# Optimization experiments

Hardware: AMD Instinct MI355X
Metric: run time of the kernel (lower is better)

Reference implementation:

```python
import jax, jax.numpy as jnp
import numpy as np

VOCAB = 50257
EMB = 512


def setup_inputs() -> dict:
    key = jax.random.key(0)
    k1, k2, k3 = jax.random.split(key, 3)
    input_token_ids = jax.random.randint(k1, (8, 4096), 0, VOCAB, dtype=jnp.int64 if jax.config.jax_enable_x64 else jnp.int32)
    W = jax.random.normal(k2, (EMB, VOCAB), dtype=jnp.float32)  # nn.Linear(vocab, emb).weight
    b = jax.random.normal(k3, (EMB,), dtype=jnp.float32)        # nn.Linear bias
    return {"input_token_ids": input_token_ids, "W": W, "b": b}


def reference(input_token_ids, W, b):
    # one_hot(ids, V) @ W.T + b  ==  W.T[ids] + b   (exact same math, gather form)
    scale = jnp.asarray(EMB, W.dtype) ** 0.5
    emb = jnp.take(W.T, input_token_ids, axis=0)  # [B, S, EMB]
    return (emb + b) * scale
```

## Files before the change

kernel.cpp:

```cpp
#include <hip/hip_runtime.h>


constexpr int VOCAB = 50257;
constexpr int EMB   = 512;
constexpr int NTOK  = 8 * 4096;
constexpr float SCALE = 22.62741699796952f;

constexpr int VB   = 256;
constexpr int NB   = (VOCAB + VB - 1) / VB;
constexpr int CAP  = 256;
constexpr int ECH  = 64;
constexpr int RSD  = VB + 1;
constexpr int SMEM_BYTES = (ECH * RSD + CAP) * 4;


__global__ __launch_bounds__(256) void build_buckets(
    const int* __restrict__ ids,
    int* __restrict__ counts,
    int* __restrict__ olist,
    int* __restrict__ buckets)
{
    int t = blockIdx.x * 256 + threadIdx.x;
    int id = ids[t];
    int bkt = id >> 8;
    int slot = atomicAdd(&counts[bkt], 1);
    if (slot < CAP) {
        buckets[bkt * CAP + slot] = (t << 8) | (id & 255);
    } else {
        int o = atomicAdd(&counts[NB], 1);
        olist[o] = t;
    }
}

__global__ __launch_bounds__(512) void scatter_main(
    const float* __restrict__ W,
    const float* __restrict__ bias,
    const int*   __restrict__ counts,
    const int*   __restrict__ buckets,
    const int*   __restrict__ olist,
    const int*   __restrict__ ids,
    float*       __restrict__ out)
{
    extern __shared__ float smem[];
    float* tile = smem;
    int*   toks = (int*)(smem + ECH * RSD);

    const int bid  = blockIdx.x;
    const int b    = bid >> 3;
    const int ec   = bid & 7;
    const int e0   = ec * ECH;
    const int tid  = threadIdx.x;
    const int lane = tid & 63;
    const int w    = tid >> 6;

    const int vstart = min(b * VB, VOCAB - VB);
    const int vadj   = b * VB - vstart;

    const int cnt = min(counts[b], CAP);
    if (tid < CAP) toks[tid] = buckets[b * CAP + tid];
    const float be = bias[e0 + lane];

    #pragma unroll
    for (int p = 0; p < 8; ++p) {
        const int r = w * 8 + p;
        const size_t rowbase = (size_t)(e0 + r) * VOCAB + vstart;
        #pragma unroll
        for (int q = 0; q < 4; ++q) {
            const float* gp = W + rowbase + q * 64 + lane;
            float* lp = &tile[r * RSD + q * 64];
            __builtin_amdgcn_global_load_lds(
                (const __attribute__((address_space(1))) void*)gp,
                (__attribute__((address_space(3))) void*)lp, 4, 0, 0);
        }
    }
    __syncthreads();

    const float* tl   = &tile[lane * RSD];
    float*       outp = out + e0 + lane;
    for (int i = w; i < cnt; i += 8) {
        const int pk = toks[i];
        const int t  = pk >> 8;
        const int vl = (pk & 255) + vadj;
        outp[(size_t)t * EMB] = (tl[vl] + be) * SCALE;
    }

    if (b == 0) {
        int n = counts[NB];
        for (int ww = w; ww < n; ww += 8) {
            int t  = olist[ww];
            int id = ids[t];
            int e  = e0 + lane;
            out[(size_t)t * EMB + e] = (W[(size_t)e * VOCAB + id] + bias[e]) * SCALE;
        }
    }
}

__global__ __launch_bounds__(256) void embed_gather(
    const int*   __restrict__ ids,
    const float* __restrict__ W,
    const float* __restrict__ b,
    float*       __restrict__ out)
{
    int idx4 = blockIdx.x * blockDim.x + threadIdx.x;
    int t    = idx4 >> 7;
    int e    = (idx4 & 127) << 2;
    int id = ids[t];
    float4 bb = *reinterpret_cast<const float4*>(b + e);
    const float* wcol = W + (size_t)id;
    float4 o;
    o.x = (wcol[(size_t)(e + 0) * VOCAB] + bb.x) * SCALE;
    o.y = (wcol[(size_t)(e + 1) * VOCAB] + bb.y) * SCALE;
    o.z = (wcol[(size_t)(e + 2) * VOCAB] + bb.z) * SCALE;
    o.w = (wcol[(size_t)(e + 3) * VOCAB] + bb.w) * SCALE;
    *reinterpret_cast<float4*>(out + (size_t)idx4 * 4) = o;
}

extern "C" void kernel_launch(void* const* d_in, const int* in_sizes, int n_in,
                              void* d_out, int out_size, void* d_ws, size_t ws_size,
                              hipStream_t stream)
{
    const int*   ids  = (const int*)  d_in[0];
    const float* W    = (const float*)d_in[1];
    const float* bias = (const float*)d_in[2];
    float*       out  = (float*)d_out;

    const size_t ws_ints_needed = (size_t)NB + 1 + NTOK + (size_t)NB * CAP;

    if (ws_size >= ws_ints_needed * sizeof(int)) {
        int* counts  = (int*)d_ws;
        int* olist   = counts + NB + 1;
        int* buckets = olist + NTOK;

        hipMemsetAsync(counts, 0, (NB + 1) * sizeof(int), stream);
        build_buckets<<<NTOK / 256, 256, 0, stream>>>(ids, counts, olist, buckets);
        scatter_main<<<NB * 8, 512, SMEM_BYTES, stream>>>(W, bias, counts, buckets,
                                                          olist, ids, out);
    } else {
        constexpr int total4 = NTOK * EMB / 4;
        embed_gather<<<total4 / 256, 256, 0, stream>>>(ids, W, bias, out);
    }
}
```

Measured before the change: 203.6 us.

## Use narrow 32-column vocab buckets with full-embedding tiles and float4 row stores

Buckets shrink from 256 to 32 vocab ids, and each block now loads all 512 embedding rows for its 32-column slice into LDS through register loads. Previously each block handled a 64-row chunk of a 256-column slice using direct global-to-LDS loads. Each token now writes its full 2KB output row as float4 stores, replacing eight scattered 256-byte writes from different blocks. This keeps the W read the same size while making output writes contiguous per token. In exchange it uses about 68KB of LDS per block, an overflow path that loops over all 512 elements, and a smaller bucket capacity of 96, which sends more tokens to the serial overflow path in block 0.

```diff
diff --git a/kernel.cpp b/kernel.cpp
--- a/kernel.cpp
+++ b/kernel.cpp
@@ -6,12 +6,12 @@
 constexpr int NTOK  = 8 * 4096;
 constexpr float SCALE = 22.62741699796952f;
 
-constexpr int VB   = 256;
+constexpr int VB   = 32;
 constexpr int NB   = (VOCAB + VB - 1) / VB;
-constexpr int CAP  = 256;
-constexpr int ECH  = 64;
-constexpr int RSD  = VB + 1;
-constexpr int SMEM_BYTES = (ECH * RSD + CAP) * 4;
+constexpr int CAP  = 96;
+constexpr int RS   = VB + 1;
+constexpr int TILE_DW = EMB * RS;
+constexpr int SMEM_BYTES = (TILE_DW + CAP) * 4;
 
 
 __global__ __launch_bounds__(256) void build_buckets(
@@ -22,10 +22,10 @@
 {
     int t = blockIdx.x * 256 + threadIdx.x;
     int id = ids[t];
-    int bkt = id >> 8;
+    int bkt = id >> 5;
     int slot = atomicAdd(&counts[bkt], 1);
     if (slot < CAP) {
-        buckets[bkt * CAP + slot] = (t << 8) | (id & 255);
+        buckets[bkt * CAP + slot] = (t << 5) | (id & 31);
     } else {
         int o = atomicAdd(&counts[NB], 1);
         olist[o] = t;
@@ -43,12 +43,9 @@
 {
     extern __shared__ float smem[];
     float* tile = smem;
-    int*   toks = (int*)(smem + ECH * RSD);
+    int*   toks = (int*)(smem + TILE_DW);
 
-    const int bid  = blockIdx.x;
-    const int b    = bid >> 3;
-    const int ec   = bid & 7;
-    const int e0   = ec * ECH;
+    const int b    = blockIdx.x;
     const int tid  = threadIdx.x;
     const int lane = tid & 63;
     const int w    = tid >> 6;
@@ -58,30 +55,46 @@
 
     const int cnt = min(counts[b], CAP);
     if (tid < CAP) toks[tid] = buckets[b * CAP + tid];
-    const float be = bias[e0 + lane];
 
+    const float4 bA = reinterpret_cast<const float4*>(bias)[lane];
+    const float4 bB = reinterpret_cast<const float4*>(bias)[64 + lane];
+
+    const int rr  = tid >> 5;
+    const int col = tid & 31;
+    float v[32];
     #pragma unroll
-    for (int p = 0; p < 8; ++p) {
-        const int r = w * 8 + p;
-        const size_t rowbase = (size_t)(e0 + r) * VOCAB + vstart;
-        #pragma unroll
-        for (int q = 0; q < 4; ++q) {
-            const float* gp = W + rowbase + q * 64 + lane;
-            float* lp = &tile[r * RSD + q * 64];
-            __builtin_amdgcn_global_load_lds(
-                (const __attribute__((address_space(1))) void*)gp,
-                (__attribute__((address_space(3))) void*)lp, 4, 0, 0);
-        }
-    }
+    for (int p = 0; p < 32; ++p)
+        v[p] = W[(size_t)(p * 16 + rr) * VOCAB + vstart + col];
+    #pragma unroll
+    for (int p = 0; p < 32; ++p)
+        tile[(p * 16 + rr) * RS + col] = v[p];
+
     __syncthreads();
 
-    const float* tl   = &tile[lane * RSD];
-    float*       outp = out + e0 + lane;
+    float4* outv = reinterpret_cast<float4*>(out);
     for (int i = w; i < cnt; i += 8) {
         const int pk = toks[i];
-        const int t  = pk >> 8;
-        const int vl = (pk & 255) + vadj;
-        outp[(size_t)t * EMB] = (tl[vl] + be) * SCALE;
+        const int t  = pk >> 5;
+        const int vl = (pk & 31) + vadj;
+        float4 oA, oB;
+        oA.x = tile[(4 * lane + 0) * RS + vl];
+        oA.y = tile[(4 * lane + 1) * RS + vl];
+        oA.z = tile[(4 * lane + 2) * RS + vl];
+        oA.w = tile[(4 * lane + 3) * RS + vl];
+        oB.x = tile[(256 + 4 * lane + 0) * RS + vl];
+        oB.y = tile[(256 + 4 * lane + 1) * RS + vl];
+        oB.z = tile[(256 + 4 * lane + 2) * RS + vl];
+        oB.w = tile[(256 + 4 * lane + 3) * RS + vl];
+        oA.x = (oA.x + bA.x) * SCALE;
+        oA.y = (oA.y + bA.y) * SCALE;
+        oA.z = (oA.z + bA.z) * SCALE;
+        oA.w = (oA.w + bA.w) * SCALE;
+        oB.x = (oB.x + bB.x) * SCALE;
+        oB.y = (oB.y + bB.y) * SCALE;
+        oB.z = (oB.z + bB.z) * SCALE;
+        oB.w = (oB.w + bB.w) * SCALE;
+        outv[(size_t)t * 128 + lane]      = oA;
+        outv[(size_t)t * 128 + 64 + lane] = oB;
     }
 
     if (b == 0) {
@@ -89,8 +102,11 @@
         for (int ww = w; ww < n; ww += 8) {
             int t  = olist[ww];
             int id = ids[t];
-            int e  = e0 + lane;
-            out[(size_t)t * EMB + e] = (W[(size_t)e * VOCAB + id] + bias[e]) * SCALE;
+            #pragma unroll
+            for (int m = 0; m < 8; ++m) {
+                int e = lane + m * 64;
+                out[(size_t)t * EMB + e] = (W[(size_t)e * VOCAB + id] + bias[e]) * SCALE;
+            }
         }
     }
 }
@@ -133,8 +149,8 @@
 
         hipMemsetAsync(counts, 0, (NB + 1) * sizeof(int), stream);
         build_buckets<<<NTOK / 256, 256, 0, stream>>>(ids, counts, olist, buckets);
-        scatter_main<<<NB * 8, 512, SMEM_BYTES, stream>>>(W, bias, counts, buckets,
-                                                          olist, ids, out);
+        scatter_main<<<NB, 512, SMEM_BYTES, stream>>>(W, bias, counts, buckets,
+                                                      olist, ids, out);
     } else {
         constexpr int total4 = NTOK * EMB / 4;
         embed_gather<<<total4 / 256, 256, 0, stream>>>(ids, W, bias, out);
```

Result: faster. 190.5 us (-6.4%).
